# Kernel optimization log

Measured on AMD Instinct MI355X. Metric: run time of the kernel, lower is better.

## Reference

```python
import jax, jax.numpy as jnp
import numpy as np

TAU = 2.0        # LIF membrane time constant
ALPHA = 4.0      # spikingjelly default Sigmoid surrogate alpha
NUM_HEADS = 8

@jax.custom_vjp
def spike(x):
    return (x >= 0.0).astype(x.dtype)

def _spike_fwd(x):
    return spike(x), x

def _spike_bwd(x, g):
    s = jax.nn.sigmoid(ALPHA * x)
    return (g * ALPHA * s * (1.0 - s),)

spike.defvjp(_spike_fwd, _spike_bwd)

def lif(x_seq, v_th):
    """Multi-step LIF over leading time dim. Hard reset to 0, detach_reset."""
    def step(v, xt):
        h = v + (xt - v) / TAU
        s = spike(h - v_th)
        v_new = h * (1.0 - jax.lax.stop_gradient(s))
        return v_new, s
    _, s_seq = jax.lax.scan(step, jnp.zeros_like(x_seq[0]), x_seq)
    return s_seq

def bn_eval(x, w, b, m, v, eps=1e-5):
    # BatchNorm1d in eval mode over channel dim C (last axis here, since the
    # torch code transposes to (TB,C,N) purely to make C the channel axis).
    inv = w / jnp.sqrt(v + eps)
    return x * inv + (b - m * inv)

def setup_inputs() -> dict:
    key = jax.random.key(0)
    T, B, N, C = 4, 8, 512, 512
    ks = jax.random.split(key, 32)
    d = {"x": jax.random.normal(ks[0], (T, B, N, C), dtype=jnp.float32)}
    names = ["q", "k", "v", "p"]
    for i, nm in enumerate(names):
        kk = jax.random.split(ks[i + 1], 6)
        d[nm + "_w"] = jax.random.normal(kk[0], (C, C), dtype=jnp.float32) * (C ** -0.5)
        d[nm + "_b"] = jax.random.normal(kk[1], (C,), dtype=jnp.float32) * 0.01
        d[nm + "_bn_w"] = jax.random.uniform(kk[2], (C,), minval=0.5, maxval=1.5, dtype=jnp.float32)
        d[nm + "_bn_b"] = jax.random.normal(kk[3], (C,), dtype=jnp.float32) * 0.1
        d[nm + "_bn_m"] = jax.random.normal(kk[4], (C,), dtype=jnp.float32) * 0.1
        d[nm + "_bn_v"] = jax.random.uniform(kk[5], (C,), minval=0.5, maxval=1.5, dtype=jnp.float32)
    return d

def _forward(x, q_w, q_b, q_bn_w, q_bn_b, q_bn_m, q_bn_v,
             k_w, k_b, k_bn_w, k_bn_b, k_bn_m, k_bn_v,
             v_w, v_b, v_bn_w, v_bn_b, v_bn_m, v_bn_v,
             p_w, p_b, p_bn_w, p_bn_b, p_bn_m, p_bn_v):
    T, B, N, C = x.shape
    H = NUM_HEADS
    hd = C // H
    scale = hd ** -0.5

    def branch(w, b, bw, bb, bm, bv):
        y = jnp.einsum("tbnc,dc->tbnd", x, w) + b            # Linear
        y = bn_eval(y, bw, bb, bm, bv)                        # BN1d (eval)
        y = lif(y, 1.0)                                       # (T,B,N,C) spikes
        return y.reshape(T, B, N, H, hd).transpose(0, 1, 3, 2, 4)  # (T,B,H,N,hd)

    q = branch(q_w, q_b, q_bn_w, q_bn_b, q_bn_m, q_bn_v)
    k = branch(k_w, k_b, k_bn_w, k_bn_b, k_bn_m, k_bn_v)
    v = branch(v_w, v_b, v_bn_w, v_bn_b, v_bn_m, v_bn_v)

    gamma = 1.0 - 2.0 ** (-5.0 - jnp.arange(H, dtype=jnp.float32))
    idx = jnp.arange(N)
    dist = jnp.abs(idx[:, None] - idx[None, :]).astype(jnp.float32)  # bidirectional
    D = gamma[:, None, None] ** dist                                  # (H,N,N)

    attn = jnp.einsum("tbhnd,tbhmd->tbhnm", q, k) * scale * D
    out = jnp.einsum("tbhnm,tbhmd->tbhnd", attn, v)
    out = out.transpose(0, 1, 3, 2, 4).reshape(T, B, N, C)
    out = lif(out, 0.5)                                      # retention_lif, v_th=0.5

    y = jnp.einsum("tbnc,dc->tbnd", out, p_w) + p_b
    y = bn_eval(y, p_bn_w, p_bn_b, p_bn_m, p_bn_v)
    return lif(y, 1.0)

def reference(x, q_w, q_b, q_bn_w, q_bn_b, q_bn_m, q_bn_v,
              k_w, k_b, k_bn_w, k_bn_b, k_bn_m, k_bn_v,
              v_w, v_b, v_bn_w, v_bn_b, v_bn_m, v_bn_v,
              p_w, p_b, p_bn_w, p_bn_b, p_bn_m, p_bn_v):
    return _forward(x, q_w, q_b, q_bn_w, q_bn_b, q_bn_m, q_bn_v,
                    k_w, k_b, k_bn_w, k_bn_b, k_bn_m, k_bn_v,
                    v_w, v_b, v_bn_w, v_bn_b, v_bn_m, v_bn_v,
                    p_w, p_b, p_bn_w, p_bn_b, p_bn_m, p_bn_v)
```

## Files before the change

### kernel.cpp

```cpp
#include <hip/hip_runtime.h>
#include <cstdint>

typedef unsigned long long u64;

#define TPB 256
#define MARGIN 5e-4
#define FCAP (1 << 20)

typedef __bf16 bf16x8 __attribute__((ext_vector_type(8)));
typedef __bf16 bf16x4 __attribute__((ext_vector_type(4)));
typedef float f32x4 __attribute__((ext_vector_type(4)));

typedef __attribute__((address_space(1))) void GV;
typedef __attribute__((address_space(3))) void LV;
typedef __attribute__((address_space(3))) char LC;

#define GLD(gsrc, ldst) __builtin_amdgcn_global_load_lds( \
    (GV*)(void*)(gsrc), (LV*)(ldst), 16, 0, 0)

__global__ void init_kernel(double* __restrict__ pw, int* __restrict__ ctr) {
    int h = threadIdx.x;
    if (h < 8) {
        double gamma = 1.0 - ldexp(1.0, -5 - h);
        double p = 1.0;
        for (int i = 0; i < 512; ++i) { pw[h * 512 + i] = p; p *= gamma; }
        ctr[h] = 0;
    }
}

__global__ void split_all(const float* __restrict__ x,
                          const float* __restrict__ w0, const float* __restrict__ w1,
                          const float* __restrict__ w2, const float* __restrict__ w3,
                          __bf16* __restrict__ Xh, __bf16* __restrict__ Xl,
                          __bf16* __restrict__ Wsp) {
    int blk = blockIdx.x;
    if (blk < 8192) {
        size_t i = (size_t)blk * 1024 + threadIdx.x * 4;
        int m = (int)(i >> 9), c = (int)(i & 511);
        int mp = (m & 4095) * 4 + (m >> 12);
        float4 v = *(const float4*)(x + i);
        bf16x4 h4, l4;
        #pragma unroll
        for (int e = 0; e < 4; ++e) {
            float f = (&v.x)[e];
            __bf16 hh = (__bf16)f;
            h4[e] = hh;
            l4[e] = (__bf16)(f - (float)hh);
        }
        size_t dst = (size_t)mp * 512 + c;
        *(bf16x4*)(Xh + dst) = h4;
        *(bf16x4*)(Xl + dst) = l4;
    } else {
        int wb = blk - 8192;
        int br = wb >> 8;
        const float* ws[4] = {w0, w1, w2, w3};
        const float* src = ws[br];
        __bf16* hi = Wsp + (size_t)br * 524288;
        __bf16* lo = hi + 262144;
        size_t i = (size_t)(wb & 255) * 1024 + threadIdx.x * 4;
        float4 v = *(const float4*)(src + i);
        bf16x4 h4, l4;
        #pragma unroll
        for (int e = 0; e < 4; ++e) {
            float f = (&v.x)[e];
            __bf16 hh = (__bf16)f;
            h4[e] = hh;
            l4[e] = (__bf16)(f - (float)hh);
        }
        *(bf16x4*)(hi + i) = h4;
        *(bf16x4*)(lo + i) = l4;
    }
}

__global__ __launch_bounds__(256) void gemm_lif_mask(
    const __bf16* __restrict__ Ahg, const __bf16* __restrict__ Alg,
    const __bf16* __restrict__ Whg, const __bf16* __restrict__ Wlg,
    const float* __restrict__ bias,
    const float* __restrict__ bnw, const float* __restrict__ bnb,
    const float* __restrict__ bnm, const float* __restrict__ bnv,
    u64* __restrict__ msk, int* __restrict__ ctr, int* __restrict__ list, int slot)
{
    __shared__ __bf16 AhS[2][128][32];
    __shared__ __bf16 AlS[2][128][32];
    __shared__ __bf16 WhS[2][128][32];
    __shared__ __bf16 WlS[2][128][32];

    const int tid = threadIdx.x;
    const int m0 = blockIdx.x * 128;
    const int d0 = blockIdx.y * 128;
    const int wv = tid >> 6;
    const int wm = wv >> 1;
    const int wd = wv & 1;
    const int lane = tid & 63;
    const int fr = lane & 15;
    const int fg = lane >> 4;

    const int lr   = lane >> 2;
    const int csrc = (lane & 3) ^ ((lane >> 3) & 3);
    const int rA0  = wv * 32 + lr;
    const __bf16* gAh0 = Ahg + (size_t)(m0 + rA0) * 512 + csrc * 8;
    const __bf16* gAh1 = gAh0 + (size_t)16 * 512;
    const __bf16* gAl0 = Alg + (size_t)(m0 + rA0) * 512 + csrc * 8;
    const __bf16* gAl1 = gAl0 + (size_t)16 * 512;
    const __bf16* gWh0 = Whg + (size_t)(d0 + rA0) * 512 + csrc * 8;
    const __bf16* gWh1 = gWh0 + (size_t)16 * 512;
    const __bf16* gWl0 = Wlg + (size_t)(d0 + rA0) * 512 + csrc * 8;
    const __bf16* gWl1 = gWl0 + (size_t)16 * 512;

    unsigned ldsOff = __builtin_amdgcn_readfirstlane((unsigned)(wv * 2048));
    LC* lAh = (LC*)(LV*)&AhS[0][0][0] + ldsOff;
    LC* lAl = (LC*)(LV*)&AlS[0][0][0] + ldsOff;
    LC* lWh = (LC*)(LV*)&WhS[0][0][0] + ldsOff;
    LC* lWl = (LC*)(LV*)&WlS[0][0][0] + ldsOff;

    const int fcol = (fg ^ ((fr >> 1) & 3)) * 16;

    f32x4 acc[4][4];
    #pragma unroll
    for (int i = 0; i < 4; ++i)
        #pragma unroll
        for (int j = 0; j < 4; ++j)
            acc[i][j] = (f32x4){0.f, 0.f, 0.f, 0.f};

    GLD(gAh0, lAh); GLD(gAh1, lAh + 1024);
    GLD(gAl0, lAl); GLD(gAl1, lAl + 1024);
    GLD(gWh0, lWh); GLD(gWh1, lWh + 1024);
    GLD(gWl0, lWl); GLD(gWl1, lWl + 1024);

    #pragma unroll
    for (int kk = 0; kk < 16; ++kk) {
        const int k0 = kk * 32;
        const int cur = kk & 1;
        const int nxt = cur ^ 1;
        __syncthreads();
        if (kk < 15) {
            GLD(gAh0 + k0 + 32, lAh + nxt * 8192); GLD(gAh1 + k0 + 32, lAh + nxt * 8192 + 1024);
            GLD(gAl0 + k0 + 32, lAl + nxt * 8192); GLD(gAl1 + k0 + 32, lAl + nxt * 8192 + 1024);
            GLD(gWh0 + k0 + 32, lWh + nxt * 8192); GLD(gWh1 + k0 + 32, lWh + nxt * 8192 + 1024);
            GLD(gWl0 + k0 + 32, lWl + nxt * 8192); GLD(gWl1 + k0 + 32, lWl + nxt * 8192 + 1024);
        }

        bf16x8 ah[4], bh[4], bl[4];
        #pragma unroll
        for (int i = 0; i < 4; ++i) {
            int row = wm * 64 + i * 16 + fr;
            ah[i] = *(const bf16x8*)((const char*)&AhS[cur][0][0] + row * 64 + fcol);
        }
        #pragma unroll
        for (int j = 0; j < 4; ++j) {
            int row = wd * 64 + j * 16 + fr;
            bh[j] = *(const bf16x8*)((const char*)&WhS[cur][0][0] + row * 64 + fcol);
            bl[j] = *(const bf16x8*)((const char*)&WlS[cur][0][0] + row * 64 + fcol);
        }
        #pragma unroll
        for (int i = 0; i < 4; ++i)
            #pragma unroll
            for (int j = 0; j < 4; ++j) {
                acc[i][j] = __builtin_amdgcn_mfma_f32_16x16x32_bf16(ah[i], bh[j], acc[i][j], 0, 0, 0);
                acc[i][j] = __builtin_amdgcn_mfma_f32_16x16x32_bf16(ah[i], bl[j], acc[i][j], 0, 0, 0);
            }
        bf16x8 al[4];
        #pragma unroll
        for (int i = 0; i < 4; ++i) {
            int row = wm * 64 + i * 16 + fr;
            al[i] = *(const bf16x8*)((const char*)&AlS[cur][0][0] + row * 64 + fcol);
        }
        #pragma unroll
        for (int i = 0; i < 4; ++i)
            #pragma unroll
            for (int j = 0; j < 4; ++j)
                acc[i][j] = __builtin_amdgcn_mfma_f32_16x16x32_bf16(al[i], bh[j], acc[i][j], 0, 0, 0);
    }

    double invj[4], shj[4], bsj[4];
    #pragma unroll
    for (int j = 0; j < 4; ++j) {
        int d = d0 + wd * 64 + j * 16 + fr;
        invj[j] = (double)bnw[d] / sqrt((double)bnv[d] + 1e-5);
        shj[j]  = (double)bnb[d] - (double)bnm[d] * invj[j];
        bsj[j]  = (double)bias[d];
    }
    int hword = (d0 >> 6) + wd;
    int bn0 = blockIdx.x * 32 + wm * 16;

    #pragma unroll
    for (int i = 0; i < 4; ++i) {
        int bn = bn0 + i * 4 + fg;
        int b = bn >> 9, n = bn & 511;
        u64 w[4] = {0ull, 0ull, 0ull, 0ull};
        #pragma unroll
        for (int j = 0; j < 4; ++j) {
            double v = 0.0;
            bool fl = false;
            #pragma unroll
            for (int t = 0; t < 4; ++t) {
                double y = ((double)acc[i][j][t] + bsj[j]) * invj[j] + shj[j];
                double hh = v + (y - v) * 0.5;
                fl |= fabs(hh - 1.0) < MARGIN;
                bool s = hh >= 1.0;
                u64 blt = __ballot(s);
                w[t] |= ((blt >> (fg * 16)) & 0xFFFFull) << (j * 16);
                v = s ? 0.0 : hh;
            }
            if (fl) {
                int d = d0 + wd * 64 + j * 16 + fr;
                int idx = atomicAdd(ctr + slot, 1);
                if (idx < FCAP) list[idx] = (b << 18) | (n << 9) | d;
            }
        }
        if (fr == 0) {
            #pragma unroll
            for (int t = 0; t < 4; ++t)
                msk[((t * 8 + b) * 8 + hword) * 512 + n] = w[t];
        }
    }
}

__global__ __launch_bounds__(256) void gemm_final_lif(
    const __bf16* __restrict__ Ahg,
    const __bf16* __restrict__ Whg, const __bf16* __restrict__ Wlg,
    const float* __restrict__ bias,
    const float* __restrict__ bnw, const float* __restrict__ bnb,
    const float* __restrict__ bnm, const float* __restrict__ bnv,
    float* __restrict__ out, int* __restrict__ ctr, int* __restrict__ list)
{
    __shared__ __bf16 AhS[2][128][32];
    __shared__ __bf16 WhS[2][128][32];
    __shared__ __bf16 WlS[2][128][32];

    const int tid = threadIdx.x;
    const int m0 = blockIdx.x * 128;
    const int d0 = blockIdx.y * 128;
    const int wv = tid >> 6;
    const int wm = wv >> 1;
    const int wd = wv & 1;
    const int lane = tid & 63;
    const int fr = lane & 15;
    const int fg = lane >> 4;

    const int lr   = lane >> 2;
    const int csrc = (lane & 3) ^ ((lane >> 3) & 3);
    const int rA0  = wv * 32 + lr;
    const __bf16* gAh0 = Ahg + (size_t)(m0 + rA0) * 512 + csrc * 8;
    const __bf16* gAh1 = gAh0 + (size_t)16 * 512;
    const __bf16* gWh0 = Whg + (size_t)(d0 + rA0) * 512 + csrc * 8;
    const __bf16* gWh1 = gWh0 + (size_t)16 * 512;
    const __bf16* gWl0 = Wlg + (size_t)(d0 + rA0) * 512 + csrc * 8;
    const __bf16* gWl1 = gWl0 + (size_t)16 * 512;

    unsigned ldsOff = __builtin_amdgcn_readfirstlane((unsigned)(wv * 2048));
    LC* lAh = (LC*)(LV*)&AhS[0][0][0] + ldsOff;
    LC* lWh = (LC*)(LV*)&WhS[0][0][0] + ldsOff;
    LC* lWl = (LC*)(LV*)&WlS[0][0][0] + ldsOff;

    const int fcol = (fg ^ ((fr >> 1) & 3)) * 16;

    f32x4 acc[4][4];
    #pragma unroll
    for (int i = 0; i < 4; ++i)
        #pragma unroll
        for (int j = 0; j < 4; ++j)
            acc[i][j] = (f32x4){0.f, 0.f, 0.f, 0.f};

    GLD(gAh0, lAh); GLD(gAh1, lAh + 1024);
    GLD(gWh0, lWh); GLD(gWh1, lWh + 1024);
    GLD(gWl0, lWl); GLD(gWl1, lWl + 1024);

    #pragma unroll
    for (int kk = 0; kk < 16; ++kk) {
        const int k0 = kk * 32;
        const int cur = kk & 1;
        const int nxt = cur ^ 1;
        __syncthreads();
        if (kk < 15) {
            GLD(gAh0 + k0 + 32, lAh + nxt * 8192); GLD(gAh1 + k0 + 32, lAh + nxt * 8192 + 1024);
            GLD(gWh0 + k0 + 32, lWh + nxt * 8192); GLD(gWh1 + k0 + 32, lWh + nxt * 8192 + 1024);
            GLD(gWl0 + k0 + 32, lWl + nxt * 8192); GLD(gWl1 + k0 + 32, lWl + nxt * 8192 + 1024);
        }

        bf16x8 ah[4], bh[4], bl[4];
        #pragma unroll
        for (int i = 0; i < 4; ++i) {
            int row = wm * 64 + i * 16 + fr;
            ah[i] = *(const bf16x8*)((const char*)&AhS[cur][0][0] + row * 64 + fcol);
        }
        #pragma unroll
        for (int j = 0; j < 4; ++j) {
            int row = wd * 64 + j * 16 + fr;
            bh[j] = *(const bf16x8*)((const char*)&WhS[cur][0][0] + row * 64 + fcol);
            bl[j] = *(const bf16x8*)((const char*)&WlS[cur][0][0] + row * 64 + fcol);
        }
        #pragma unroll
        for (int i = 0; i < 4; ++i)
            #pragma unroll
            for (int j = 0; j < 4; ++j) {
                acc[i][j] = __builtin_amdgcn_mfma_f32_16x16x32_bf16(ah[i], bh[j], acc[i][j], 0, 0, 0);
                acc[i][j] = __builtin_amdgcn_mfma_f32_16x16x32_bf16(ah[i], bl[j], acc[i][j], 0, 0, 0);
            }
    }

    double invj[4], shj[4], bsj[4];
    #pragma unroll
    for (int j = 0; j < 4; ++j) {
        int d = d0 + wd * 64 + j * 16 + fr;
        invj[j] = (double)bnw[d] / sqrt((double)bnv[d] + 1e-5);
        shj[j]  = (double)bnb[d] - (double)bnm[d] * invj[j];
        bsj[j]  = (double)bias[d];
    }
    int bn0 = blockIdx.x * 32 + wm * 16;

    #pragma unroll
    for (int i = 0; i < 4; ++i) {
        int bn = bn0 + i * 4 + fg;
        int b = bn >> 9, n = bn & 511;
        #pragma unroll
        for (int j = 0; j < 4; ++j) {
            int d = d0 + wd * 64 + j * 16 + fr;
            double v = 0.0;
            bool fl = false;
            #pragma unroll
            for (int t = 0; t < 4; ++t) {
                double y = ((double)acc[i][j][t] + bsj[j]) * invj[j] + shj[j];
                double hh = v + (y - v) * 0.5;
                fl |= fabs(hh - 1.0) < MARGIN;
                bool s = hh >= 1.0;
                out[((size_t)((t * 8 + b) * 512 + n) << 9) + d] = s ? 1.0f : 0.0f;
                v = s ? 0.0 : hh;
            }
            if (fl) {
                int idx = atomicAdd(ctr + 3, 1);
                if (idx < FCAP) list[idx] = (b << 18) | (n << 9) | d;
            }
        }
    }
}

__global__ void fix_mask(const float* __restrict__ x, const float* __restrict__ w,
                         const float* __restrict__ bias,
                         const float* __restrict__ bnw, const float* __restrict__ bnb,
                         const float* __restrict__ bnm, const float* __restrict__ bnv,
                         u64* __restrict__ msk, const int* __restrict__ ctr,
                         const int* __restrict__ list, int slot) {
    int cnt = ctr[slot]; if (cnt > FCAP) cnt = FCAP;
    int wv = (blockIdx.x * blockDim.x + threadIdx.x) >> 6;
    int nw = (gridDim.x * blockDim.x) >> 6;
    int lane = threadIdx.x & 63;
    for (int i = wv; i < cnt; i += nw) {
        int g = list[i];
        int c = g & 511, n = (g >> 9) & 511, b = g >> 18;
        int h = c >> 6;
        const float* wr = w + (size_t)c * 512;
        double dot[4];
        #pragma unroll
        for (int t = 0; t < 4; ++t) {
            const float* xr = x + ((size_t)((t * 8 + b) * 512 + n) << 9);
            double p = 0.0;
            #pragma unroll
            for (int j = 0; j < 8; ++j)
                p += (double)xr[lane + 64 * j] * (double)wr[lane + 64 * j];
            dot[t] = p;
        }
        #pragma unroll
        for (int off = 32; off; off >>= 1) {
            #pragma unroll
            for (int t = 0; t < 4; ++t)
                dot[t] += __shfl_xor(dot[t], off, 64);
        }
        if (lane == 0) {
            double inv = (double)bnw[c] / sqrt((double)bnv[c] + 1e-5);
            double sh  = (double)bnb[c] - (double)bnm[c] * inv;
            double bs  = (double)bias[c];
            double v = 0.0;
            u64 bit = 1ull << (c & 63);
            for (int t = 0; t < 4; ++t) {
                double y = (dot[t] + bs) * inv + sh;
                double hh = v + (y - v) * 0.5;
                bool s = hh >= 1.0;
                u64* wp_ = &msk[((t * 8 + b) * 8 + h) * 512 + n];
                if (s) atomicOr(wp_, bit); else atomicAnd(wp_, ~bit);
                v = s ? 0.0 : hh;
            }
        }
    }
}

__global__ __launch_bounds__(256) void ret_fused2(
    const u64* __restrict__ qm, const u64* __restrict__ km,
    const u64* __restrict__ vm, const double* __restrict__ pw,
    float* __restrict__ O)
{
    int bid = blockIdx.x;
    int tbh = bid >> 3;
    int n0 = (bid & 7) * 64;
    int h = tbh & 7;
    int tb = tbh >> 3;
    int tid = threadIdx.x;
    int wv = tid >> 6, lane = tid & 63, fr = lane & 15, fg = lane >> 4;
    int wn = wv * 16;

    __shared__ __bf16 Ks[64][72];
    __shared__ u64 VsTg[16][66];
    __shared__ u64 ShTg[4][16][17];
    __shared__ u64 SlTg[4][16][17];
    __shared__ u64 vmc[64];
    __shared__ float pwf[512];

    int base = tbh * 512;
    for (int i = tid; i < 512; i += 256) pwf[i] = (float)pw[h * 512 + i] * 0.125f;

    union U8 { u64 q[2]; bf16x8 v; };

    u64 qw = qm[base + n0 + wn + fr];
    bf16x8 qf[2];
    #pragma unroll
    for (int ks = 0; ks < 2; ++ks) {
        int e0 = ks * 32 + fg * 8;
        u64 plo = 0, phi = 0;
        #pragma unroll
        for (int e = 0; e < 4; ++e) {
            if ((qw >> (e0 + e)) & 1ull)     plo |= 0x3F80ull << (16 * e);
            if ((qw >> (e0 + 4 + e)) & 1ull) phi |= 0x3F80ull << (16 * e);
        }
        U8 u; u.q[0] = plo; u.q[1] = phi; qf[ks] = u.v;
    }

    f32x4 acc_o[4];
    #pragma unroll
    for (int j = 0; j < 4; ++j) acc_o[j] = (f32x4){0.f, 0.f, 0.f, 0.f};

    int nglob = n0 + wn + fr;

    for (int mc = 0; mc < 8; ++mc) {
        __syncthreads();
        {
            int row = tid >> 2, q4 = (tid & 3) * 16;
            u64 kw = km[base + mc * 64 + row];
            #pragma unroll
            for (int s = 0; s < 4; ++s) {
                int e0 = q4 + s * 4;
                u64 pk = 0;
                #pragma unroll
                for (int e = 0; e < 4; ++e)
                    if ((kw >> (e0 + e)) & 1ull) pk |= 0x3F80ull << (16 * e);
                *(u64*)&Ks[row][e0] = pk;
            }
        }
        if (tid < 64) vmc[tid] = vm[base + mc * 64 + tid];
        __syncthreads();
        {
            #pragma unroll
            for (int c = 0; c < 4; ++c) {
                int mg = wv * 4 + c;
                u64 pk = 0;
                #pragma unroll
                for (int e = 0; e < 4; ++e)
                    if ((vmc[mg * 4 + e] >> lane) & 1ull) pk |= 0x3F80ull << (16 * e);
                VsTg[mg][lane] = pk;
            }
        }
        f32x4 accs[4];
        #pragma unroll
        for (int j = 0; j < 4; ++j) accs[j] = (f32x4){0.f, 0.f, 0.f, 0.f};
        #pragma unroll
        for (int ks = 0; ks < 2; ++ks) {
            #pragma unroll
            for (int j = 0; j < 4; ++j) {
                bf16x8 ka = *(const bf16x8*)&Ks[j * 16 + fr][ks * 32 + fg * 8];
                accs[j] = __builtin_amdgcn_mfma_f32_16x16x32_bf16(ka, qf[ks], accs[j], 0, 0, 0);
            }
        }
        #pragma unroll
        for (int j = 0; j < 4; ++j) {
            u64 ph = 0, pl = 0;
            #pragma unroll
            for (int reg = 0; reg < 4; ++reg) {
                int m = mc * 64 + j * 16 + fg * 4 + reg;
                int dist = nglob - m; if (dist < 0) dist = -dist;
                float a = accs[j][reg] * pwf[dist];
                unsigned ab = __builtin_bit_cast(unsigned, a);
                unsigned hb = ab & 0xFFFF0000u;
                float lp = a - __builtin_bit_cast(float, hb);
                __bf16 lpb = (__bf16)lp;
                ph |= (u64)(ab >> 16) << (16 * reg);
                pl |= (u64)__builtin_bit_cast(unsigned short, lpb) << (16 * reg);
            }
            ShTg[wv][j * 4 + fg][fr] = ph;
            SlTg[wv][j * 4 + fg][fr] = pl;
        }
        __syncthreads();
        #pragma unroll
        for (int ks2 = 0; ks2 < 2; ++ks2) {
            int mga = ks2 * 8 + fg * 2;
            U8 ua, ul;
            ua.q[0] = ShTg[wv][mga][fr];  ua.q[1] = ShTg[wv][mga + 1][fr];
            ul.q[0] = SlTg[wv][mga][fr];  ul.q[1] = SlTg[wv][mga + 1][fr];
            #pragma unroll
            for (int j2 = 0; j2 < 4; ++j2) {
                U8 uv;
                uv.q[0] = VsTg[mga][j2 * 16 + fr];
                uv.q[1] = VsTg[mga + 1][j2 * 16 + fr];
                acc_o[j2] = __builtin_amdgcn_mfma_f32_16x16x32_bf16(ua.v, uv.v, acc_o[j2], 0, 0, 0);
                acc_o[j2] = __builtin_amdgcn_mfma_f32_16x16x32_bf16(ul.v, uv.v, acc_o[j2], 0, 0, 0);
            }
        }
    }

    #pragma unroll
    for (int j2 = 0; j2 < 4; ++j2) {
        int c = h * 64 + j2 * 16 + fr;
        #pragma unroll
        for (int reg = 0; reg < 4; ++reg) {
            int n = n0 + wn + fg * 4 + reg;
            O[((size_t)(tb * 512 + n) << 9) + c] = acc_o[j2][reg];
        }
    }
}

__global__ void lif_ret_bf2(const float* __restrict__ Y, __bf16* __restrict__ Rb,
                            int* __restrict__ ctr, int* __restrict__ list) {
    int g = blockIdx.x * TPB + threadIdx.x;
    int c = g & 511, n = (g >> 9) & 511, b = g >> 18;
    size_t pbase = ((size_t)(b * 512 + n) * 4) * 512 + c;
    double v = 0.0, eb = 0.0;
    bool flag = false;
    for (int t = 0; t < 4; ++t) {
        size_t idx = ((size_t)((t * 8 + b) * 512 + n) << 9) + c;
        double x = (double)Y[idx];
        double hh = v + (x - v) * 0.5;
        eb = 0.5 * eb + 0.5 * (fabs(x) * 1e-4);
        flag |= fabs(hh - 0.5) <= eb + 1e-9;
        bool s = hh >= 0.5;
        Rb[pbase + (size_t)t * 512] = s ? (__bf16)1.0f : (__bf16)0.0f;
        v = s ? 0.0 : hh;
        if (s) eb = 0.0;
    }
    if (flag) {
        int i2 = atomicAdd(ctr + 4, 1);
        if (i2 < FCAP) list[i2] = g;
    }
}

__global__ void repair_ret_bf2(const u64* __restrict__ qm, const u64* __restrict__ km,
                               const u64* __restrict__ vm, const double* __restrict__ pw,
                               const int* __restrict__ ctr, const int* __restrict__ list,
                               __bf16* __restrict__ Rb) {
    int cnt = ctr[4]; if (cnt > FCAP) cnt = FCAP;
    int wv = (blockIdx.x * blockDim.x + threadIdx.x) >> 6;
    int nw = (gridDim.x * blockDim.x) >> 6;
    int lane = threadIdx.x & 63;
    for (int i = wv; i < cnt; i += nw) {
        int g = list[i];
        int c = g & 511, n = (g >> 9) & 511, b = g >> 18;
        int h = c >> 6, d = c & 63;
        double acc_t[4];
        for (int t = 0; t < 4; ++t) {
            int base = ((t * 8 + b) * 8 + h) * 512;
            u64 qw = qm[base + n];
            double p = 0.0;
            for (int j = 0; j < 8; ++j) {
                int m = j * 64 + lane;
                u64 kk = km[base + m];
                u64 vvm = vm[base + m];
                if ((vvm >> d) & 1ull) {
                    int dist = n - m; if (dist < 0) dist = -dist;
                    p += (double)__popcll(qw & kk) * pw[h * 512 + dist];
                }
            }
            acc_t[t] = p;
        }
        #pragma unroll
        for (int off = 32; off; off >>= 1) {
            #pragma unroll
            for (int t = 0; t < 4; ++t) acc_t[t] += __shfl_xor(acc_t[t], off, 64);
        }
        if (lane == 0) {
            double v = 0.0;
            size_t pbase = ((size_t)(b * 512 + n) * 4) * 512 + c;
            for (int t = 0; t < 4; ++t) {
                double x = acc_t[t] * 0.125;
                double hh = v + (x - v) * 0.5;
                bool s = hh >= 0.5;
                Rb[pbase + (size_t)t * 512] = s ? (__bf16)1.0f : (__bf16)0.0f;
                v = s ? 0.0 : hh;
            }
        }
    }
}

__global__ void fix_final_direct(const __bf16* __restrict__ rr, const float* __restrict__ w,
                                 const float* __restrict__ bias,
                                 const float* __restrict__ bnw, const float* __restrict__ bnb,
                                 const float* __restrict__ bnm, const float* __restrict__ bnv,
                                 const int* __restrict__ ctr, const int* __restrict__ list,
                                 float* __restrict__ out) {
    int cnt = ctr[3]; if (cnt > FCAP) cnt = FCAP;
    int wv = (blockIdx.x * blockDim.x + threadIdx.x) >> 6;
    int nw = (gridDim.x * blockDim.x) >> 6;
    int lane = threadIdx.x & 63;
    for (int i = wv; i < cnt; i += nw) {
        int g = list[i];
        int c = g & 511, n = (g >> 9) & 511, b = g >> 18;
        const float* wr = w + (size_t)c * 512;
        double dot[4];
        #pragma unroll
        for (int t = 0; t < 4; ++t) {
            const __bf16* xr = rr + ((size_t)(b * 512 + n) * 4 + t) * 512;
            double p = 0.0;
            #pragma unroll
            for (int j = 0; j < 8; ++j)
                p += (double)(float)xr[lane + 64 * j] * (double)wr[lane + 64 * j];
            dot[t] = p;
        }
        #pragma unroll
        for (int off = 32; off; off >>= 1) {
            #pragma unroll
            for (int t = 0; t < 4; ++t)
                dot[t] += __shfl_xor(dot[t], off, 64);
        }
        if (lane == 0) {
            double inv = (double)bnw[c] / sqrt((double)bnv[c] + 1e-5);
            double sh  = (double)bnb[c] - (double)bnm[c] * inv;
            double bs  = (double)bias[c];
            double v = 0.0;
            for (int t = 0; t < 4; ++t) {
                double y = (dot[t] + bs) * inv + sh;
                double hh = v + (y - v) * 0.5;
                bool s = hh >= 1.0;
                out[((size_t)((t * 8 + b) * 512 + n) << 9) + c] = s ? 1.0f : 0.0f;
                v = s ? 0.0 : hh;
            }
        }
    }
}

__global__ __launch_bounds__(256) void gemm_bn_mfma(
    const float* __restrict__ A, const float* __restrict__ W,
    const float* __restrict__ bias,
    const float* __restrict__ bnw, const float* __restrict__ bnb,
    const float* __restrict__ bnm, const float* __restrict__ bnv,
    float* __restrict__ out)
{
    __shared__ __bf16 Ah[128][36];
    __shared__ __bf16 Al[128][36];
    __shared__ __bf16 Wh[64][36];
    __shared__ __bf16 Wl[64][36];

    const int tid = threadIdx.x;
    const int m0 = blockIdx.x * 128;
    const int d0 = blockIdx.y * 64;
    const int wv = tid >> 6;
    const int wm = wv >> 1;
    const int wd = wv & 1;
    const int lane = tid & 63;
    const int fr = lane & 15;
    const int fg = lane >> 4;
    const int srow = tid >> 3;
    const int scol = (tid & 7) * 4;

    f32x4 acc[4][2];
    #pragma unroll
    for (int i = 0; i < 4; ++i)
        #pragma unroll
        for (int j = 0; j < 2; ++j)
            acc[i][j] = (f32x4){0.f, 0.f, 0.f, 0.f};

    for (int k0 = 0; k0 < 512; k0 += 32) {
        __syncthreads();
        #pragma unroll
        for (int rep = 0; rep < 4; ++rep) {
            int row = srow + 32 * rep;
            float4 va = *(const float4*)(A + (size_t)(m0 + row) * 512 + k0 + scol);
            #pragma unroll
            for (int e = 0; e < 4; ++e) {
                float f = (&va.x)[e];
                __bf16 h = (__bf16)f;
                Ah[row][scol + e] = h;
                Al[row][scol + e] = (__bf16)(f - (float)h);
            }
        }
        #pragma unroll
        for (int rep = 0; rep < 2; ++rep) {
            int row = srow + 32 * rep;
            float4 vw = *(const float4*)(W + (size_t)(d0 + row) * 512 + k0 + scol);
            #pragma unroll
            for (int e = 0; e < 4; ++e) {
                float f = (&vw.x)[e];
                __bf16 h = (__bf16)f;
                Wh[row][scol + e] = h;
                Wl[row][scol + e] = (__bf16)(f - (float)h);
            }
        }
        __syncthreads();

        union FU { bf16x8 v8; struct { __bf16 a[4], b[4]; } s; };
        bf16x8 ah[4], al[4], bh[2], bl[2];
        #pragma unroll
        for (int i = 0; i < 4; ++i) {
            int row = wm * 64 + i * 16 + fr;
            FU u1, u2;
            *(double*)&u1.s.a[0] = *(const double*)&Ah[row][fg * 8];
            *(double*)&u1.s.b[0] = *(const double*)&Ah[row][fg * 8 + 4];
            *(double*)&u2.s.a[0] = *(const double*)&Al[row][fg * 8];
            *(double*)&u2.s.b[0] = *(const double*)&Al[row][fg * 8 + 4];
            ah[i] = u1.v8; al[i] = u2.v8;
        }
        #pragma unroll
        for (int j = 0; j < 2; ++j) {
            int row = wd * 32 + j * 16 + fr;
            FU u1, u2;
            *(double*)&u1.s.a[0] = *(const double*)&Wh[row][fg * 8];
            *(double*)&u1.s.b[0] = *(const double*)&Wh[row][fg * 8 + 4];
            *(double*)&u2.s.a[0] = *(const double*)&Wl[row][fg * 8];
            *(double*)&u2.s.b[0] = *(const double*)&Wl[row][fg * 8 + 4];
            bh[j] = u1.v8; bl[j] = u2.v8;
        }
        #pragma unroll
        for (int i = 0; i < 4; ++i)
            #pragma unroll
            for (int j = 0; j < 2; ++j) {
                acc[i][j] = __builtin_amdgcn_mfma_f32_16x16x32_bf16(ah[i], bh[j], acc[i][j], 0, 0, 0);
                acc[i][j] = __builtin_amdgcn_mfma_f32_16x16x32_bf16(ah[i], bl[j], acc[i][j], 0, 0, 0);
                acc[i][j] = __builtin_amdgcn_mfma_f32_16x16x32_bf16(al[i], bh[j], acc[i][j], 0, 0, 0);
            }
    }

    #pragma unroll
    for (int j = 0; j < 2; ++j) {
        int d = d0 + wd * 32 + j * 16 + fr;
        double inv = (double)bnw[d] / sqrt((double)bnv[d] + 1e-5);
        double sh  = (double)bnb[d] - (double)bnm[d] * inv;
        double bs  = (double)bias[d];
        #pragma unroll
        for (int i = 0; i < 4; ++i) {
            #pragma unroll
            for (int reg = 0; reg < 4; ++reg) {
                int m = m0 + wm * 64 + i * 16 + fg * 4 + reg;
                out[(size_t)m * 512 + d] = (float)(((double)acc[i][j][reg] + bs) * inv + sh);
            }
        }
    }
}

__global__ void lif_mask_flag(const float* __restrict__ Y, u64* __restrict__ msk,
                              int* __restrict__ ctr, int* __restrict__ list, int slot) {
    int g = blockIdx.x * TPB + threadIdx.x;
    int c = g & 511, n = (g >> 9) & 511, b = g >> 18;
    int h = c >> 6;
    int lane = threadIdx.x & 63;
    double v = 0.0;
    bool flag = false;
    for (int t = 0; t < 4; ++t) {
        float y = Y[((size_t)((t * 8 + b) * 512 + n) << 9) + c];
        double hh = v + ((double)y - v) * 0.5;
        flag |= fabs(hh - 1.0) < MARGIN;
        bool s = hh >= 1.0;
        u64 mk = __ballot(s);
        if (lane == 0) msk[((t * 8 + b) * 8 + h) * 512 + n] = mk;
        v = s ? 0.0 : hh;
    }
    if (flag) {
        int idx = atomicAdd(ctr + slot, 1);
        if (idx < FCAP) list[idx] = g;
    }
}

__global__ void lif_ret_f(const float* __restrict__ Y, float* __restrict__ R,
                          int* __restrict__ ctr, int* __restrict__ list) {
    int g = blockIdx.x * TPB + threadIdx.x;
    int c = g & 511, n = (g >> 9) & 511, b = g >> 18;
    double v = 0.0, eb = 0.0;
    bool flag = false;
    for (int t = 0; t < 4; ++t) {
        size_t idx = ((size_t)((t * 8 + b) * 512 + n) << 9) + c;
        double x = (double)Y[idx];
        double hh = v + (x - v) * 0.5;
        eb = 0.5 * eb + 0.5 * (fabs(x) * 1e-4);
        flag |= fabs(hh - 0.5) <= eb + 1e-9;
        bool s = hh >= 0.5;
        R[idx] = s ? 1.0f : 0.0f;
        v = s ? 0.0 : hh;
        if (s) eb = 0.0;
    }
    if (flag) {
        int i2 = atomicAdd(ctr + 4, 1);
        if (i2 < FCAP) list[i2] = g;
    }
}

__global__ void repair_ret_f(const u64* __restrict__ qm, const u64* __restrict__ km,
                             const u64* __restrict__ vm, const double* __restrict__ pw,
                             const int* __restrict__ ctr, const int* __restrict__ list,
                             float* __restrict__ r) {
    int cnt = ctr[4]; if (cnt > FCAP) cnt = FCAP;
    int wv = (blockIdx.x * blockDim.x + threadIdx.x) >> 6;
    int nw = (gridDim.x * blockDim.x) >> 6;
    int lane = threadIdx.x & 63;
    for (int i = wv; i < cnt; i += nw) {
        int g = list[i];
        int c = g & 511, n = (g >> 9) & 511, b = g >> 18;
        int h = c >> 6, d = c & 63;
        double acc_t[4];
        for (int t = 0; t < 4; ++t) {
            int base = ((t * 8 + b) * 8 + h) * 512;
            u64 qw = qm[base + n];
            double p = 0.0;
            for (int j = 0; j < 8; ++j) {
                int m = j * 64 + lane;
                u64 kk = km[base + m];
                u64 vvm = vm[base + m];
                if ((vvm >> d) & 1ull) {
                    int dist = n - m; if (dist < 0) dist = -dist;
                    p += (double)__popcll(qw & kk) * pw[h * 512 + dist];
                }
            }
            acc_t[t] = p;
        }
        #pragma unroll
        for (int off = 32; off; off >>= 1) {
            #pragma unroll
            for (int t = 0; t < 4; ++t) acc_t[t] += __shfl_xor(acc_t[t], off, 64);
        }
        if (lane == 0) {
            double v = 0.0;
            for (int t = 0; t < 4; ++t) {
                double x = acc_t[t] * 0.125;
                double hh = v + (x - v) * 0.5;
                bool s = hh >= 0.5;
                r[((size_t)((t * 8 + b) * 512 + n) << 9) + c] = s ? 1.0f : 0.0f;
                v = s ? 0.0 : hh;
            }
        }
    }
}

__global__ void final_flag(const float* __restrict__ Y, int* __restrict__ ctr,
                           int* __restrict__ list) {
    int g = blockIdx.x * TPB + threadIdx.x;
    int c = g & 511, n = (g >> 9) & 511, b = g >> 18;
    double v = 0.0;
    bool flag = false;
    for (int t = 0; t < 4; ++t) {
        float y = Y[((size_t)((t * 8 + b) * 512 + n) << 9) + c];
        double hh = v + ((double)y - v) * 0.5;
        flag |= fabs(hh - 1.0) < MARGIN;
        bool s = hh >= 1.0;
        v = s ? 0.0 : hh;
    }
    if (flag) {
        int idx = atomicAdd(ctr + 3, 1);
        if (idx < FCAP) list[idx] = g;
    }
}

__global__ void fix_final_f(const float* __restrict__ rr, const float* __restrict__ w,
                            const float* __restrict__ bias,
                            const float* __restrict__ bnw, const float* __restrict__ bnb,
                            const float* __restrict__ bnm, const float* __restrict__ bnv,
                            const int* __restrict__ ctr, int* __restrict__ list) {
    int cnt = ctr[3]; if (cnt > FCAP) cnt = FCAP;
    int wv = (blockIdx.x * blockDim.x + threadIdx.x) >> 6;
    int nw = (gridDim.x * blockDim.x) >> 6;
    int lane = threadIdx.x & 63;
    for (int i = wv; i < cnt; i += nw) {
        int g = list[i] & 0x00FFFFFF;
        int c = g & 511, n = (g >> 9) & 511, b = g >> 18;
        const float* wr = w + (size_t)c * 512;
        double dot[4];
        #pragma unroll
        for (int t = 0; t < 4; ++t) {
            const float* xr = rr + ((size_t)((t * 8 + b) * 512 + n) << 9);
            double p = 0.0;
            #pragma unroll
            for (int j = 0; j < 8; ++j)
                p += (double)xr[lane + 64 * j] * (double)wr[lane + 64 * j];
            dot[t] = p;
        }
        #pragma unroll
        for (int off = 32; off; off >>= 1) {
            #pragma unroll
            for (int t = 0; t < 4; ++t)
                dot[t] += __shfl_xor(dot[t], off, 64);
        }
        if (lane == 0) {
            double inv = (double)bnw[c] / sqrt((double)bnv[c] + 1e-5);
            double sh  = (double)bnb[c] - (double)bnm[c] * inv;
            double bs  = (double)bias[c];
            double v = 0.0;
            int sp = 0;
            for (int t = 0; t < 4; ++t) {
                double y = (dot[t] + bs) * inv + sh;
                double hh = v + (y - v) * 0.5;
                bool s = hh >= 1.0;
                sp |= (s ? 1 : 0) << t;
                v = s ? 0.0 : hh;
            }
            list[i] = g | (sp << 24);
        }
    }
}

__global__ void final_write(const float* __restrict__ Y, float* __restrict__ out) {
    int g = blockIdx.x * TPB + threadIdx.x;
    int c = g & 511, n = (g >> 9) & 511, b = g >> 18;
    double v = 0.0;
    for (int t = 0; t < 4; ++t) {
        size_t idx = ((size_t)((t * 8 + b) * 512 + n) << 9) + c;
        float y = Y[idx];
        double hh = v + ((double)y - v) * 0.5;
        bool s = hh >= 1.0;
        out[idx] = s ? 1.0f : 0.0f;
        v = s ? 0.0 : hh;
    }
}

__global__ void fix_scatter(const int* __restrict__ ctr, const int* __restrict__ list,
                            float* __restrict__ out) {
    int cnt = ctr[3]; if (cnt > FCAP) cnt = FCAP;
    int i = blockIdx.x * blockDim.x + threadIdx.x;
    if (i >= cnt) return;
    int e = list[i];
    int g = e & 0x00FFFFFF, sp = (e >> 24) & 0xF;
    int c = g & 511, n = (g >> 9) & 511, b = g >> 18;
    for (int t = 0; t < 4; ++t)
        out[((size_t)((t * 8 + b) * 512 + n) << 9) + c] = ((sp >> t) & 1) ? 1.0f : 0.0f;
}

extern "C" void kernel_launch(void* const* d_in, const int* in_sizes, int n_in,
                              void* d_out, int out_size, void* d_ws, size_t ws_size,
                              hipStream_t stream) {
    const float* x = (const float*)d_in[0];
    const float *w[4], *bi[4], *bnw[4], *bnb[4], *bnm[4], *bnv[4];
    for (int br = 0; br < 4; ++br) {
        int base = 1 + br * 6;
        w[br]   = (const float*)d_in[base + 0];
        bi[br]  = (const float*)d_in[base + 1];
        bnw[br] = (const float*)d_in[base + 2];
        bnb[br] = (const float*)d_in[base + 3];
        bnm[br] = (const float*)d_in[base + 4];
        bnv[br] = (const float*)d_in[base + 5];
    }

    const size_t NX = (size_t)16384 * 512;
    char* p = (char*)d_ws;
    double* pw = (double*)p;  p += 8 * 512 * sizeof(double);
    u64* qm = (u64*)p;        p += 131072 * sizeof(u64);
    u64* km = (u64*)p;        p += 131072 * sizeof(u64);
    u64* vm = (u64*)p;        p += 131072 * sizeof(u64);
    int* ctr = (int*)p;       p += 1024;
    int* list = (int*)p;      p += (size_t)FCAP * sizeof(int);
    float* Y = (float*)p;     p += NX * 4;
    __bf16* Xh = (__bf16*)p;  p += NX * 2;
    __bf16* Xl = (__bf16*)p;  p += NX * 2;
    __bf16* Wsp = (__bf16*)p; p += (size_t)4 * 2 * 262144 * 2;
    size_t need_fast = (size_t)(p - (char*)d_ws);
    int fast = ws_size >= need_fast;

    init_kernel<<<1, 64, 0, stream>>>(pw, ctr);

    dim3 g2(128, 4);
    dim3 gg(128, 8);

    if (fast) {
        split_all<<<8192 + 1024, 256, 0, stream>>>(x, w[0], w[1], w[2], w[3], Xh, Xl, Wsp);
        for (int br = 0; br < 3; ++br) {
            u64* msk = br == 0 ? qm : (br == 1 ? km : vm);
            gemm_lif_mask<<<g2, 256, 0, stream>>>(Xh, Xl,
                Wsp + (size_t)br * 524288, Wsp + (size_t)br * 524288 + 262144,
                bi[br], bnw[br], bnb[br], bnm[br], bnv[br], msk, ctr, list, br);
            fix_mask<<<128, 256, 0, stream>>>(x, w[br], bi[br], bnw[br], bnb[br],
                                              bnm[br], bnv[br], msk, ctr, list, br);
        }
        ret_fused2<<<2048, 256, 0, stream>>>(qm, km, vm, pw, Y);
        lif_ret_bf2<<<8192, TPB, 0, stream>>>(Y, Xh, ctr, list);
        repair_ret_bf2<<<256, 256, 0, stream>>>(qm, km, vm, pw, ctr, list, Xh);
        gemm_final_lif<<<g2, 256, 0, stream>>>(Xh,
            Wsp + (size_t)3 * 524288, Wsp + (size_t)3 * 524288 + 262144,
            bi[3], bnw[3], bnb[3], bnm[3], bnv[3], (float*)d_out, ctr, list);
        fix_final_direct<<<128, 256, 0, stream>>>(Xh, w[3], bi[3], bnw[3], bnb[3],
                                                  bnm[3], bnv[3], ctr, list, (float*)d_out);
    } else {
        for (int br = 0; br < 3; ++br) {
            u64* msk = br == 0 ? qm : (br == 1 ? km : vm);
            gemm_bn_mfma<<<gg, 256, 0, stream>>>(x, w[br], bi[br], bnw[br], bnb[br],
                                                 bnm[br], bnv[br], Y);
            lif_mask_flag<<<8192, TPB, 0, stream>>>(Y, msk, ctr, list, br);
            fix_mask<<<128, 256, 0, stream>>>(x, w[br], bi[br], bnw[br], bnb[br],
                                              bnm[br], bnv[br], msk, ctr, list, br);
        }
        float* r = (float*)d_out;
        ret_fused2<<<2048, 256, 0, stream>>>(qm, km, vm, pw, Y);
        lif_ret_f<<<8192, TPB, 0, stream>>>(Y, r, ctr, list);
        repair_ret_f<<<256, 256, 0, stream>>>(qm, km, vm, pw, ctr, list, r);
        gemm_bn_mfma<<<gg, 256, 0, stream>>>(r, w[3], bi[3], bnw[3], bnb[3],
                                             bnm[3], bnv[3], Y);
        final_flag<<<8192, TPB, 0, stream>>>(Y, ctr, list);
        fix_final_f<<<128, 256, 0, stream>>>(r, w[3], bi[3], bnw[3], bnb[3],
                                             bnm[3], bnv[3], ctr, list);
        final_write<<<8192, TPB, 0, stream>>>(Y, (float*)d_out);
        fix_scatter<<<4096, 256, 0, stream>>>(ctr, list, (float*)d_out);
    }
}
```

Before: 269.6 us.

## Pre-expand K/V masks to bf16 and double-buffer async LDS loads in retention

A new expand_kv kernel turns the K and V bitmasks into dense bf16 tiles once, with V stored transposed, in a buffer that reuses the Y workspace. The retention kernel then streams these tiles into double-buffered, XOR-swizzled shared memory using global_load_lds. The next chunk is prefetched while the current one is computed, and one barrier per iteration is dropped. This removes the bit-expansion work that every block used to repeat for the same K and V data. In exchange it adds an extra kernel launch and more global and L2 traffic, and the retention output now goes directly to d_out.

New measurement: 275.9 us. 2.3% more time.

```diff
diff --git a/kernel.cpp b/kernel.cpp
--- a/kernel.cpp
+++ b/kernel.cpp
@@ -384,9 +384,50 @@
     }
 }
 
-__global__ __launch_bounds__(256) void ret_fused2(
-    const u64* __restrict__ qm, const u64* __restrict__ km,
-    const u64* __restrict__ vm, const double* __restrict__ pw,
+__global__ void expand_kv(const u64* __restrict__ km, const u64* __restrict__ vm,
+                          __bf16* __restrict__ Kb, __bf16* __restrict__ VbT) {
+    int tbh = blockIdx.x;
+    int tid = threadIdx.x;
+    int base = tbh * 512;
+
+    #pragma unroll 2
+    for (int pass = 0; pass < 16; ++pass) {
+        int row = pass * 32 + (tid >> 3);
+        u64 kw = km[base + row];
+        int e0 = (tid & 7) * 8;
+        u64 lo = 0, hi = 0;
+        #pragma unroll
+        for (int e = 0; e < 4; ++e) {
+            if ((kw >> (e0 + e)) & 1ull)     lo |= 0x3F80ull << (16 * e);
+            if ((kw >> (e0 + 4 + e)) & 1ull) hi |= 0x3F80ull << (16 * e);
+        }
+        u64* dst = (u64*)(Kb + ((size_t)(tbh * 512 + row)) * 64 + e0);
+        dst[0] = lo; dst[1] = hi;
+    }
+
+    __shared__ u64 vmc[64];
+    for (int mc = 0; mc < 8; ++mc) {
+        __syncthreads();
+        if (tid < 64) vmc[tid] = vm[base + mc * 64 + tid];
+        __syncthreads();
+        int d = tid >> 2, mseg = (tid & 3) * 16;
+        u64 q[4];
+        #pragma unroll
+        for (int s4 = 0; s4 < 4; ++s4) {
+            u64 pk = 0;
+            #pragma unroll
+            for (int e = 0; e < 4; ++e)
+                if ((vmc[mseg + s4 * 4 + e] >> d) & 1ull) pk |= 0x3F80ull << (16 * e);
+            q[s4] = pk;
+        }
+        u64* dst = (u64*)(VbT + ((size_t)(tbh * 64 + d)) * 512 + mc * 64 + mseg);
+        dst[0] = q[0]; dst[1] = q[1]; dst[2] = q[2]; dst[3] = q[3];
+    }
+}
+
+__global__ __launch_bounds__(256) void ret_fused3(
+    const u64* __restrict__ qm, const __bf16* __restrict__ Kb,
+    const __bf16* __restrict__ VbT, const double* __restrict__ pw,
     float* __restrict__ O)
 {
     int bid = blockIdx.x;
@@ -398,11 +439,10 @@
     int wv = tid >> 6, lane = tid & 63, fr = lane & 15, fg = lane >> 4;
     int wn = wv * 16;
 
-    __shared__ __bf16 Ks[64][72];
-    __shared__ u64 VsTg[16][66];
+    __shared__ __bf16 Ks[2][64][64];
+    __shared__ __bf16 Vb[2][64][64];
     __shared__ u64 ShTg[4][16][17];
     __shared__ u64 SlTg[4][16][17];
-    __shared__ u64 vmc[64];
     __shared__ float pwf[512];
 
     int base = tbh * 512;
@@ -424,40 +464,29 @@
         U8 u; u.q[0] = plo; u.q[1] = phi; qf[ks] = u.v;
     }
 
+    const int srcRow = wv * 8 + (lane >> 3);
+    const int srcGr  = (lane & 7) ^ (lane >> 3);
+    const __bf16* gK = Kb + ((size_t)(tbh * 512 + srcRow)) * 64 + srcGr * 8;
+    const __bf16* gV = VbT + ((size_t)(tbh * 64 + srcRow)) * 512 + srcGr * 8;
+
+    unsigned ldsW = __builtin_amdgcn_readfirstlane((unsigned)(wv * 1024));
+    LC* lK = (LC*)(LV*)&Ks[0][0][0] + ldsW;
+    LC* lV = (LC*)(LV*)&Vb[0][0][0] + ldsW;
+
+    GLD(gK, lK);               GLD(gK + 2048, lK + 4096);
+    GLD(gV, lV);               GLD(gV + 32 * 512, lV + 4096);
+
     f32x4 acc_o[4];
     #pragma unroll
     for (int j = 0; j < 4; ++j) acc_o[j] = (f32x4){0.f, 0.f, 0.f, 0.f};
 
     int nglob = n0 + wn + fr;
+    const int swz = (fr & 7) * 16;
 
     for (int mc = 0; mc < 8; ++mc) {
+        const int cur = mc & 1, nxt = cur ^ 1;
         __syncthreads();
-        {
-            int row = tid >> 2, q4 = (tid & 3) * 16;
-            u64 kw = km[base + mc * 64 + row];
-            #pragma unroll
-            for (int s = 0; s < 4; ++s) {
-                int e0 = q4 + s * 4;
-                u64 pk = 0;
-                #pragma unroll
-                for (int e = 0; e < 4; ++e)
-                    if ((kw >> (e0 + e)) & 1ull) pk |= 0x3F80ull << (16 * e);
-                *(u64*)&Ks[row][e0] = pk;
-            }
-        }
-        if (tid < 64) vmc[tid] = vm[base + mc * 64 + tid];
-        __syncthreads();
-        {
-            #pragma unroll
-            for (int c = 0; c < 4; ++c) {
-                int mg = wv * 4 + c;
-                u64 pk = 0;
-                #pragma unroll
-                for (int e = 0; e < 4; ++e)
-                    if ((vmc[mg * 4 + e] >> lane) & 1ull) pk |= 0x3F80ull << (16 * e);
-                VsTg[mg][lane] = pk;
-            }
-        }
+
         f32x4 accs[4];
         #pragma unroll
         for (int j = 0; j < 4; ++j) accs[j] = (f32x4){0.f, 0.f, 0.f, 0.f};
@@ -465,7 +494,9 @@
         for (int ks = 0; ks < 2; ++ks) {
             #pragma unroll
             for (int j = 0; j < 4; ++j) {
-                bf16x8 ka = *(const bf16x8*)&Ks[j * 16 + fr][ks * 32 + fg * 8];
+                int row = j * 16 + fr;
+                bf16x8 ka = *(const bf16x8*)((const char*)&Ks[cur][0][0]
+                              + row * 128 + (((ks * 4 + fg) * 16) ^ swz));
                 accs[j] = __builtin_amdgcn_mfma_f32_16x16x32_bf16(ka, qf[ks], accs[j], 0, 0, 0);
             }
         }
@@ -488,6 +519,14 @@
             SlTg[wv][j * 4 + fg][fr] = pl;
         }
         __syncthreads();
+
+        if (mc < 7) {
+            const __bf16* gk2 = gK + (mc + 1) * 4096;
+            const __bf16* gv2 = gV + (mc + 1) * 64;
+            GLD(gk2, lK + nxt * 8192);            GLD(gk2 + 2048, lK + nxt * 8192 + 4096);
+            GLD(gv2, lV + nxt * 8192);            GLD(gv2 + 32 * 512, lV + nxt * 8192 + 4096);
+        }
+
         #pragma unroll
         for (int ks2 = 0; ks2 < 2; ++ks2) {
             int mga = ks2 * 8 + fg * 2;
@@ -496,11 +535,11 @@
             ul.q[0] = SlTg[wv][mga][fr];  ul.q[1] = SlTg[wv][mga + 1][fr];
             #pragma unroll
             for (int j2 = 0; j2 < 4; ++j2) {
-                U8 uv;
-                uv.q[0] = VsTg[mga][j2 * 16 + fr];
-                uv.q[1] = VsTg[mga + 1][j2 * 16 + fr];
-                acc_o[j2] = __builtin_amdgcn_mfma_f32_16x16x32_bf16(ua.v, uv.v, acc_o[j2], 0, 0, 0);
-                acc_o[j2] = __builtin_amdgcn_mfma_f32_16x16x32_bf16(ul.v, uv.v, acc_o[j2], 0, 0, 0);
+                int vrow = j2 * 16 + fr;
+                bf16x8 vb = *(const bf16x8*)((const char*)&Vb[cur][0][0]
+                              + vrow * 128 + (((ks2 * 4 + fg) * 16) ^ swz));
+                acc_o[j2] = __builtin_amdgcn_mfma_f32_16x16x32_bf16(ua.v, vb, acc_o[j2], 0, 0, 0);
+                acc_o[j2] = __builtin_amdgcn_mfma_f32_16x16x32_bf16(ul.v, vb, acc_o[j2], 0, 0, 0);
             }
         }
     }
@@ -764,20 +803,20 @@
     }
 }
 
-__global__ void lif_ret_f(const float* __restrict__ Y, float* __restrict__ R,
-                          int* __restrict__ ctr, int* __restrict__ list) {
+__global__ void lif_ret_f(float* __restrict__ YR, int* __restrict__ ctr,
+                          int* __restrict__ list) {
     int g = blockIdx.x * TPB + threadIdx.x;
     int c = g & 511, n = (g >> 9) & 511, b = g >> 18;
     double v = 0.0, eb = 0.0;
     bool flag = false;
     for (int t = 0; t < 4; ++t) {
         size_t idx = ((size_t)((t * 8 + b) * 512 + n) << 9) + c;
-        double x = (double)Y[idx];
+        double x = (double)YR[idx];
         double hh = v + (x - v) * 0.5;
         eb = 0.5 * eb + 0.5 * (fabs(x) * 1e-4);
         flag |= fabs(hh - 0.5) <= eb + 1e-9;
         bool s = hh >= 0.5;
-        R[idx] = s ? 1.0f : 0.0f;
+        YR[idx] = s ? 1.0f : 0.0f;
         v = s ? 0.0 : hh;
         if (s) eb = 0.0;
     }
@@ -949,6 +988,8 @@
     int* ctr = (int*)p;       p += 1024;
     int* list = (int*)p;      p += (size_t)FCAP * sizeof(int);
     float* Y = (float*)p;     p += NX * 4;
+    __bf16* Kb  = (__bf16*)Y;
+    __bf16* VbT = Kb + (size_t)256 * 512 * 64;
     __bf16* Xh = (__bf16*)p;  p += NX * 2;
     __bf16* Xl = (__bf16*)p;  p += NX * 2;
     __bf16* Wsp = (__bf16*)p; p += (size_t)4 * 2 * 262144 * 2;
@@ -970,8 +1011,9 @@
             fix_mask<<<128, 256, 0, stream>>>(x, w[br], bi[br], bnw[br], bnb[br],
                                               bnm[br], bnv[br], msk, ctr, list, br);
         }
-        ret_fused2<<<2048, 256, 0, stream>>>(qm, km, vm, pw, Y);
-        lif_ret_bf2<<<8192, TPB, 0, stream>>>(Y, Xh, ctr, list);
+        expand_kv<<<256, 256, 0, stream>>>(km, vm, Kb, VbT);
+        ret_fused3<<<2048, 256, 0, stream>>>(qm, Kb, VbT, pw, (float*)d_out);
+        lif_ret_bf2<<<8192, TPB, 0, stream>>>((float*)d_out, Xh, ctr, list);
         repair_ret_bf2<<<256, 256, 0, stream>>>(qm, km, vm, pw, ctr, list, Xh);
         gemm_final_lif<<<g2, 256, 0, stream>>>(Xh,
             Wsp + (size_t)3 * 524288, Wsp + (size_t)3 * 524288 + 262144,
@@ -988,8 +1030,9 @@
                                               bnm[br], bnv[br], msk, ctr, list, br);
         }
         float* r = (float*)d_out;
-        ret_fused2<<<2048, 256, 0, stream>>>(qm, km, vm, pw, Y);
-        lif_ret_f<<<8192, TPB, 0, stream>>>(Y, r, ctr, list);
+        expand_kv<<<256, 256, 0, stream>>>(km, vm, Kb, VbT);
+        ret_fused3<<<2048, 256, 0, stream>>>(qm, Kb, VbT, pw, r);
+        lif_ret_f<<<8192, TPB, 0, stream>>>(r, ctr, list);
         repair_ret_f<<<256, 256, 0, stream>>>(qm, km, vm, pw, ctr, list, r);
         gemm_bn_mfma<<<gg, 256, 0, stream>>>(r, w[3], bi[3], bnw[3], bnb[3],
                                              bnm[3], bnv[3], Y);
```
